# Kernel optimization log

Hardware: AMD Instinct MI355X
Metric: run time of the kernel (lower is better)

Reference implementation:

```python
import jax, jax.numpy as jnp
import numpy as np

N = 100000   # nodes
E = 400000   # edges
G = 1024     # graphs in batch
IN = 4; H = 128; HD = 4; DH = H // HD; L = 3; ED = 4; FF = 2 * H; JK = H * L
SCALE = 1.0 / np.sqrt(DH).astype(np.float32)


def _ln(x, g, b):
    m = x.mean(-1, keepdims=True)
    v = x.var(-1, keepdims=True)
    return (x - m) / jnp.sqrt(v + 1e-5) * g + b


def setup_inputs() -> dict:
    key = jax.random.key(0)
    ks = jax.random.split(key, 24)
    rn = lambda k, s, sc=0.05: jax.random.normal(k, s, jnp.float32) * sc
    return {
        "x": rn(ks[0], (N, IN), 1.0),
        "edge_index": jax.random.randint(ks[1], (2, E), 0, N),
        "edge_attr": rn(ks[2], (E, ED), 1.0),
        "batch": jnp.sort(jax.random.randint(ks[3], (N,), 0, G)),
        "u": rn(ks[4], (G, 1), 1.0),
        "Win": rn(ks[5], (IN, H)), "b_in": jnp.zeros(H),
        "Wq": rn(ks[6], (L, H, H)), "bq": jnp.zeros((L, H)),
        "Wk": rn(ks[7], (L, H, H)), "bk": jnp.zeros((L, H)),
        "Wv": rn(ks[8], (L, H, H)), "bv": jnp.zeros((L, H)),
        "We": rn(ks[9], (L, ED, H)),
        "Wskip": rn(ks[10], (L, H, H)), "bskip": jnp.zeros((L, H)),
        "ln1_g": jnp.ones((L, H)), "ln1_b": jnp.zeros((L, H)),
        "Wf1": rn(ks[11], (L, H, FF)), "bf1": jnp.zeros((L, FF)),
        "Wf2": rn(ks[12], (L, FF, H)), "bf2": jnp.zeros((L, H)),
        "ln2_g": jnp.ones((L, H)), "ln2_b": jnp.zeros((L, H)),
        "Wg1": rn(ks[13], (JK, H)), "bg1": jnp.zeros(H),
        "Wg2": rn(ks[14], (H, 1)), "bg2": jnp.zeros(1),
        "Wh1": rn(ks[15], (JK + 1, H)), "bh1": jnp.zeros(H),
        "Wh2": rn(ks[16], (H, 3)), "bh2": jnp.zeros(3),
    }


def reference(x, edge_index, edge_attr, batch, u,
              Win, b_in, Wq, bq, Wk, bk, Wv, bv, We, Wskip, bskip,
              ln1_g, ln1_b, Wf1, bf1, Wf2, bf2, ln2_g, ln2_b,
              Wg1, bg1, Wg2, bg2, Wh1, bh1, Wh2, bh2):
    src, dst = edge_index[0], edge_index[1]
    h = x @ Win + b_in                                   # [N,H]
    xs = []
    for l in range(L):
        q = (h @ Wq[l] + bq[l]).reshape(N, HD, DH)
        k_n = h @ Wk[l] + bk[l]
        v_n = h @ Wv[l] + bv[l]
        e = edge_attr @ We[l]                            # [E,H] edge bias
        ke = (k_n[src] + e).reshape(E, HD, DH)
        ve = (v_n[src] + e).reshape(E, HD, DH)
        logits = (q[dst] * ke).sum(-1) * SCALE           # [E,HD]
        m = jax.ops.segment_max(logits, dst, N)
        p = jnp.exp(logits - m[dst])
        s = jax.ops.segment_sum(p, dst, N)
        alpha = p / (s[dst] + 1e-16)                     # segment softmax per dst node
        agg = jax.ops.segment_sum(alpha[:, :, None] * ve, dst, N).reshape(N, H)
        attn = agg + h @ Wskip[l] + bskip[l]             # root weight (skip lin)
        h = _ln(h + attn, ln1_g[l], ln1_b[l])
        ff = jax.nn.relu(h @ Wf1[l] + bf1[l]) @ Wf2[l] + bf2[l]
        h = _ln(h + ff, ln2_g[l], ln2_b[l])
        xs.append(h)
    xc = jnp.concatenate(xs, -1)                         # JumpingKnowledge 'cat' [N,JK]
    gate = (jax.nn.relu(xc @ Wg1 + bg1) @ Wg2 + bg2)[:, 0]  # [N]
    gm = jax.ops.segment_max(gate, batch, G)
    gp = jnp.exp(gate - gm[batch])
    gs = jax.ops.segment_sum(gp, batch, G)
    w = gp / (gs[batch] + 1e-16)                         # per-graph softmax
    pooled = jax.ops.segment_sum(w[:, None] * xc, batch, G)  # [G,JK]
    out = jnp.concatenate([pooled, u], 1)                # [G,JK+1]
    return jax.nn.relu(out @ Wh1 + bh1) @ Wh2 + bh2      # [G,3]
```

## Files before the change

### kernel.cpp

```cpp
#include <hip/hip_runtime.h>
#include <math.h>

#define H 128
#define LAYERS 3
#define FFDIM 256
#define JK 384
#define ATT_SCALE 0.17677669529663687f

typedef unsigned short u16;
typedef __attribute__((ext_vector_type(4))) float f32x4;
typedef __attribute__((ext_vector_type(8))) short short8;
typedef __attribute__((ext_vector_type(8))) unsigned short ushort8v;

static inline int cdiv(int a, int b) { return (a + b - 1) / b; }

static __device__ __forceinline__ float bf2f(u16 u) {
    union { unsigned int i; float f; } v; v.i = ((unsigned int)u) << 16; return v.f;
}
static __device__ __forceinline__ u16 f2bf(float f) {
    union { float f; unsigned int i; } v; v.f = f;
    unsigned int r = v.i + 0x7FFFu + ((v.i >> 16) & 1u);
    return (u16)(r >> 16);
}

__global__ void hist_kernel(const int* __restrict__ ei, int* __restrict__ counts, int E) {
    int e = blockIdx.x * blockDim.x + threadIdx.x;
    if (e >= E) return;
    atomicAdd(&counts[ei[E + e]], 1);
}

__global__ __launch_bounds__(256) void scan1_kernel(const int* __restrict__ counts,
                                                    int* __restrict__ offsets,
                                                    int* __restrict__ bsum, int N) {
    __shared__ int sh[256];
    int t = threadIdx.x;
    int base = blockIdx.x * 1024 + t * 4;
    int v0 = 0, v1 = 0, v2 = 0, v3 = 0;
    if (base + 3 < N) {
        int4 q = *(const int4*)&counts[base];
        v0 = q.x; v1 = q.y; v2 = q.z; v3 = q.w;
    } else {
        if (base < N) v0 = counts[base];
        if (base + 1 < N) v1 = counts[base + 1];
        if (base + 2 < N) v2 = counts[base + 2];
        if (base + 3 < N) v3 = counts[base + 3];
    }
    int ts = v0 + v1 + v2 + v3;
    sh[t] = ts; __syncthreads();
    for (int off = 1; off < 256; off <<= 1) {
        int x = (t >= off) ? sh[t - off] : 0;
        __syncthreads(); sh[t] += x; __syncthreads();
    }
    int excl = sh[t] - ts;
    if (base < N)     offsets[base]     = excl;
    if (base + 1 < N) offsets[base + 1] = excl + v0;
    if (base + 2 < N) offsets[base + 2] = excl + v0 + v1;
    if (base + 3 < N) offsets[base + 3] = excl + v0 + v1 + v2;
    if (t == 255) bsum[blockIdx.x] = sh[255];
}

__global__ __launch_bounds__(128) void scan2_kernel(const int* __restrict__ bsum,
                                                    int* __restrict__ boffs,
                                                    int* __restrict__ offsets, int nb, int N) {
    __shared__ int sh[128];
    int t = threadIdx.x;
    int s = (t < nb) ? bsum[t] : 0;
    sh[t] = s; __syncthreads();
    for (int off = 1; off < 128; off <<= 1) {
        int x = (t >= off) ? sh[t - off] : 0;
        __syncthreads(); sh[t] += x; __syncthreads();
    }
    if (t < nb) boffs[t] = sh[t] - s;
    if (t == 0) offsets[N] = sh[nb - 1];
}

__global__ __launch_bounds__(256) void scan3_kernel(int* __restrict__ offsets,
                                                    const int* __restrict__ boffs, int N) {
    int add = boffs[blockIdx.x];
    int base = blockIdx.x * 1024 + threadIdx.x * 4;
#pragma unroll
    for (int i = 0; i < 4; ++i)
        if (base + i < N) offsets[base + i] += add;
}

__global__ void scatter_kernel(const int* __restrict__ ei, const float* __restrict__ eattr,
                               const int* __restrict__ offsets,
                               int* __restrict__ cursor, int* __restrict__ psrc,
                               float4* __restrict__ pe, int E) {
    int e = blockIdx.x * blockDim.x + threadIdx.x;
    if (e >= E) return;
    int d = ei[E + e];
    int pos = atomicAdd(&cursor[d], 1);
    int o = offsets[d] + pos;
    psrc[o] = ei[e];
    pe[o] = *(const float4*)&eattr[(size_t)e * 4];
}

__global__ void graph_bounds_kernel(const int* __restrict__ batch, int* __restrict__ gstart,
                                    int N, int G) {
    int g = blockIdx.x * blockDim.x + threadIdx.x;
    if (g > G) return;
    int lo = 0, hi = N;
    while (lo < hi) { int mid = (lo + hi) >> 1; if (batch[mid] < g) lo = mid + 1; else hi = mid; }
    gstart[g] = lo;
}

struct TD { const float* src; int dstoff, K, N; };
struct TA { TD d[19]; };

__global__ __launch_bounds__(256) void wconv_kernel(TA a, u16* __restrict__ WT) {
    TD d = a.d[blockIdx.y];
    int i = blockIdx.x * 256 + threadIdx.x;
    int tot = d.K * d.N;
    if (i >= tot) return;
    int c = i / d.K, k = i - c * d.K;
    WT[d.dstoff + i] = f2bf(d.src[(size_t)k * d.N + c]);
}

__global__ __launch_bounds__(256) void input_proj_kernel(const float* __restrict__ x,
                                                         const float* __restrict__ Win,
                                                         const float* __restrict__ b_in,
                                                         u16* __restrict__ h, int ldh, int N) {
    int idx = blockIdx.x * 256 + threadIdx.x;
    int n = idx >> 6, c = (idx & 63) * 2;
    if (n >= N) return;
    float4 xv = *(const float4*)&x[(size_t)n * 4];
    float o0 = b_in[c]     + xv.x * Win[c]     + xv.y * Win[H + c]     + xv.z * Win[2 * H + c]     + xv.w * Win[3 * H + c];
    float o1 = b_in[c + 1] + xv.x * Win[c + 1] + xv.y * Win[H + c + 1] + xv.z * Win[2 * H + c + 1] + xv.w * Win[3 * H + c + 1];
    ushort2 s; s.x = f2bf(o0); s.y = f2bf(o1);
    *(ushort2*)&h[(size_t)n * ldh + c] = s;
}

__device__ __forceinline__ void stage_tile(const u16* __restrict__ g, int ld, int row0,
                                           int nrows, int kt, u16* __restrict__ sm, int t) {
#pragma unroll
    for (int i = 0; i < 4; ++i) {
        int f = i * 256 + t;
        int row = f >> 3, ck = f & 7;
        int n = row0 + row; if (n >= nrows) n = nrows - 1;
        uint4 v = *(const uint4*)(g + (size_t)n * ld + kt + ck * 8);
        int sw = ck ^ (row & 7);
        *(uint4*)(sm + row * 64 + sw * 8) = v;
    }
}

template <int MODE, int NBY>
__global__ __launch_bounds__(256) void gemm_mfma(
    const u16* __restrict__ A, int lda,
    const u16* __restrict__ WT, int K,
    const float* __restrict__ b0, const float* __restrict__ b1,
    const float* __restrict__ b2, const float* __restrict__ b3,
    const u16* __restrict__ resid16,
    u16* __restrict__ obf, u16* __restrict__ obf2, float* __restrict__ of32,
    int nrows)
{
    alignas(16) __shared__ char smemraw[33792];
    u16* Asm = (u16*)smemraw;
    u16* Bsm = (u16*)(smemraw + 16384);
    float* stage = (float*)smemraw;
    int t = threadIdx.x;
    int lane = t & 63, wid = t >> 6;
    int wr = wid >> 1, wc = wid & 1;

    int T = gridDim.x, id = blockIdx.x;
    int qd = T >> 3, rr = T & 7;
    int xcd = id & 7, pos = id >> 3;
    int swz = (xcd < rr ? xcd * (qd + 1) : rr * (qd + 1) + (xcd - rr) * qd) + pos;
    int by = swz & (NBY - 1);
    int row0 = (swz / NBY) * 128;

    const u16* WTb = WT + (size_t)by * 128 * K;

    f32x4 acc[4][4] = {};

    for (int kt = 0; kt < K; kt += 64) {
        stage_tile(A, lda, row0, nrows, kt, Asm, t);
        stage_tile(WTb, K, 0, 128, kt, Bsm, t);
        __syncthreads();
        int g = lane >> 4;
        int l15 = lane & 15;
#pragma unroll
        for (int kk = 0; kk < 2; ++kk) {
            int cb = kk * 4 + g;
            short8 af[4], bf[4];
#pragma unroll
            for (int mi = 0; mi < 4; ++mi) {
                int r = wr * 64 + mi * 16 + l15;
                af[mi] = *(const short8*)(Asm + r * 64 + ((cb ^ (r & 7)) * 8));
            }
#pragma unroll
            for (int nj = 0; nj < 4; ++nj) {
                int c = wc * 64 + nj * 16 + l15;
                bf[nj] = *(const short8*)(Bsm + c * 64 + ((cb ^ (c & 7)) * 8));
            }
#pragma unroll
            for (int mi = 0; mi < 4; ++mi)
#pragma unroll
                for (int nj = 0; nj < 4; ++nj)
                    acc[mi][nj] = __builtin_amdgcn_mfma_f32_16x16x32_bf16(af[mi], bf[nj], acc[mi][nj], 0, 0, 0);
        }
        __syncthreads();
    }

    int g = lane >> 4, l15 = lane & 15;

    if (MODE == 3) {
        float* gsum = (float*)Asm;
        float part[4][4];
#pragma unroll
        for (int mi = 0; mi < 4; ++mi)
#pragma unroll
            for (int r = 0; r < 4; ++r) part[mi][r] = 0.f;
#pragma unroll
        for (int nj = 0; nj < 4; ++nj) {
            int col = wc * 64 + nj * 16 + l15;
            float bb = b0[col];
            float w2 = b1[col];
#pragma unroll
            for (int mi = 0; mi < 4; ++mi)
#pragma unroll
                for (int r = 0; r < 4; ++r) {
                    float v = fmaxf(acc[mi][nj][r] + bb, 0.f);
                    part[mi][r] = fmaf(v, w2, part[mi][r]);
                }
        }
#pragma unroll
        for (int off = 1; off <= 8; off <<= 1)
#pragma unroll
            for (int mi = 0; mi < 4; ++mi)
#pragma unroll
                for (int r = 0; r < 4; ++r) part[mi][r] += __shfl_xor(part[mi][r], off);
        if (wc == 0 && l15 == 0) {
#pragma unroll
            for (int mi = 0; mi < 4; ++mi)
#pragma unroll
                for (int r = 0; r < 4; ++r)
                    gsum[wr * 64 + mi * 16 + g * 4 + r] = part[mi][r];
        }
        __syncthreads();
        if (wc == 1 && l15 == 0) {
            float bg2v = b2[0];
#pragma unroll
            for (int mi = 0; mi < 4; ++mi)
#pragma unroll
                for (int r = 0; r < 4; ++r) {
                    int lr = wr * 64 + mi * 16 + g * 4 + r;
                    int n = row0 + lr;
                    if (n < nrows) of32[n] = part[mi][r] + gsum[lr] + bg2v;
                }
        }
        return;
    }

    const float* bias;
    u16* ob = nullptr; int ldob = 384; float* of = nullptr;
    if (MODE == 0) {
        bias = (by == 0) ? b0 : (by == 1) ? b1 : (by == 2) ? b2 : b3;
        if (by < 3) ob = obf + by * 128;
        else { ob = obf2; ldob = 128; }
    } else if (MODE == 1) {
        bias = b0 + by * 128;
        ob = obf + by * 128;
    } else {
        bias = b0;
        of = of32;
    }

#pragma unroll
    for (int p = 0; p < 2; ++p) {
        if (wr == p) {
#pragma unroll
            for (int nj = 0; nj < 4; ++nj) {
                int col = wc * 64 + nj * 16 + l15;
                float bb = bias[col];
#pragma unroll
                for (int mi = 0; mi < 4; ++mi)
#pragma unroll
                    for (int r = 0; r < 4; ++r) {
                        float v = acc[mi][nj][r] + bb;
                        if (MODE == 1) v = fmaxf(v, 0.f);
                        stage[(mi * 16 + g * 4 + r) * 132 + col] = v;
                    }
            }
        }
        __syncthreads();
        if (ob) {
#pragma unroll
            for (int it = 0; it < 4; ++it) {
                int lr = it * 16 + (t >> 4);
                int gr = row0 + p * 64 + lr;
                if (gr < nrows) {
                    int c8 = l15 * 8;
                    ushort8v o;
#pragma unroll
                    for (int i = 0; i < 8; ++i) o[i] = f2bf(stage[lr * 132 + c8 + i]);
                    *(ushort8v*)&ob[(size_t)gr * ldob + c8] = o;
                }
            }
        } else {
            int l31 = t & 31;
#pragma unroll
            for (int it = 0; it < 8; ++it) {
                int lr = it * 8 + (t >> 5);
                int gr = row0 + p * 64 + lr;
                if (gr < nrows) {
                    int c4 = l31 * 4;
                    float4 v = *(float4*)&stage[lr * 132 + c4];
                    if (MODE == 2) {
                        ushort4 rv = *(const ushort4*)&resid16[(size_t)gr * 384 + c4];
                        v.x += bf2f(rv.x); v.y += bf2f(rv.y); v.z += bf2f(rv.z); v.w += bf2f(rv.w);
                    }
                    *(float4*)&of[(size_t)gr * 128 + c4] = v;
                }
            }
        }
        __syncthreads();
    }
}

__global__ __launch_bounds__(256) void attn_kernel(
    u16* __restrict__ qkv,
    const u16* __restrict__ h_in, int ld_h,
    const u16* __restrict__ skipb,
    const int* __restrict__ offsets,
    const int* __restrict__ psrc, const float4* __restrict__ pe,
    const float* __restrict__ We_l,
    const float* __restrict__ g1, const float* __restrict__ b1,
    int N)
{
    int tid = threadIdx.x;
    int grp = tid >> 4;
    int sub = tid & 15;
    int n = blockIdx.x * 16 + grp;
    if (n >= N) return;
    int d0 = sub * 8;

    float we[4][8];
#pragma unroll
    for (int aa = 0; aa < 4; ++aa) {
        float4 w0 = *(const float4*)&We_l[aa * H + d0];
        float4 w1 = *(const float4*)&We_l[aa * H + d0 + 4];
        we[aa][0] = w0.x; we[aa][1] = w0.y; we[aa][2] = w0.z; we[aa][3] = w0.w;
        we[aa][4] = w1.x; we[aa][5] = w1.y; we[aa][6] = w1.z; we[aa][7] = w1.w;
    }

    ushort8v qraw = *(const ushort8v*)&qkv[(size_t)n * JK + d0];
    float qf[8];
#pragma unroll
    for (int i = 0; i < 8; ++i) qf[i] = bf2f(qraw[i]);

    float qe[4];
#pragma unroll
    for (int aa = 0; aa < 4; ++aa) {
        float s = 0.f;
#pragma unroll
        for (int i = 0; i < 8; ++i) s = fmaf(qf[i], we[aa][i], s);
        s += __shfl_xor(s, 1);
        s += __shfl_xor(s, 2);
        qe[aa] = s;
    }

    float m = -INFINITY, ssum = 0.f;
    float a[8] = {0.f, 0.f, 0.f, 0.f, 0.f, 0.f, 0.f, 0.f};
    float ws0 = 0.f, ws1 = 0.f, ws2 = 0.f, ws3 = 0.f;
    int e0 = offsets[n], e1 = offsets[n + 1];
    for (int j = e0; j < e1; ++j) {
        int s = psrc[j];
        float4 ea = pe[j];
        const u16* srow = qkv + (size_t)s * JK;
        ushort8v kraw = *(const ushort8v*)&srow[H + d0];
        ushort8v vraw = *(const ushort8v*)&srow[2 * H + d0];
        float part = 0.f;
#pragma unroll
        for (int i = 0; i < 8; ++i) part = fmaf(qf[i], bf2f(kraw[i]), part);
        part += __shfl_xor(part, 1);
        part += __shfl_xor(part, 2);
        float logit = (part + ea.x * qe[0] + ea.y * qe[1] + ea.z * qe[2] + ea.w * qe[3]) * ATT_SCALE;
        float mn = fmaxf(m, logit);
        float corr = __expf(m - mn);
        float p = __expf(logit - mn);
        ssum = ssum * corr + p;
#pragma unroll
        for (int i = 0; i < 8; ++i) a[i] = a[i] * corr + p * bf2f(vraw[i]);
        ws0 = ws0 * corr + p * ea.x;
        ws1 = ws1 * corr + p * ea.y;
        ws2 = ws2 * corr + p * ea.z;
        ws3 = ws3 * corr + p * ea.w;
        m = mn;
    }
    float inv = 1.f / (ssum + 1e-16f);
#pragma unroll
    for (int i = 0; i < 8; ++i)
        a[i] += ws0 * we[0][i] + ws1 * we[1][i] + ws2 * we[2][i] + ws3 * we[3][i];

    ushort8v hraw = *(const ushort8v*)&h_in[(size_t)n * ld_h + d0];
    ushort8v skraw = *(const ushort8v*)&skipb[(size_t)n * H + d0];
    float tv[8], sum = 0.f, sq = 0.f;
#pragma unroll
    for (int i = 0; i < 8; ++i) {
        tv[i] = bf2f(hraw[i]) + a[i] * inv + bf2f(skraw[i]);
        sum += tv[i]; sq += tv[i] * tv[i];
    }
#pragma unroll
    for (int off = 1; off <= 8; off <<= 1) { sum += __shfl_xor(sum, off); sq += __shfl_xor(sq, off); }
    float mean = sum * (1.f / 128.f);
    float var = sq * (1.f / 128.f) - mean * mean;
    float rstd = rsqrtf(var + 1e-5f);
    float4 ga = *(const float4*)&g1[d0];
    float4 gb = *(const float4*)&g1[d0 + 4];
    float4 ba = *(const float4*)&b1[d0];
    float4 bb = *(const float4*)&b1[d0 + 4];
    float gg[8] = {ga.x, ga.y, ga.z, ga.w, gb.x, gb.y, gb.z, gb.w};
    float bbv[8] = {ba.x, ba.y, ba.z, ba.w, bb.x, bb.y, bb.z, bb.w};
    ushort8v obv;
#pragma unroll
    for (int i = 0; i < 8; ++i)
        obv[i] = f2bf((tv[i] - mean) * rstd * gg[i] + bbv[i]);
    *(ushort8v*)&qkv[(size_t)n * JK + d0] = obv;
}

__global__ __launch_bounds__(256) void ln_kernel(const float* __restrict__ in,
                                                 const float* __restrict__ g,
                                                 const float* __restrict__ b,
                                                 u16* __restrict__ out, int ldo, int N) {
    int wid = threadIdx.x >> 6;
    int lane = threadIdx.x & 63;
    int n = blockIdx.x * 4 + wid;
    if (n >= N) return;
    int d0 = lane * 2;
    float2 t = *(const float2*)&in[(size_t)n * H + d0];
    float sum = t.x + t.y, sq = t.x * t.x + t.y * t.y;
#pragma unroll
    for (int off = 32; off; off >>= 1) { sum += __shfl_xor(sum, off); sq += __shfl_xor(sq, off); }
    float mean = sum * (1.f / 128.f);
    float var = sq * (1.f / 128.f) - mean * mean;
    float rstd = rsqrtf(var + 1e-5f);
    ushort2 s;
    s.x = f2bf((t.x - mean) * rstd * g[d0] + b[d0]);
    s.y = f2bf((t.y - mean) * rstd * g[d0 + 1] + b[d0 + 1]);
    *(ushort2*)&out[(size_t)n * ldo + d0] = s;
}

#define PCH 512
__global__ __launch_bounds__(256) void pool_kernel(const float* __restrict__ gate,
                                                   const u16* __restrict__ xc,
                                                   const int* __restrict__ gstart,
                                                   const float* __restrict__ u,
                                                   float* __restrict__ pooled, int G) {
    int g = blockIdx.x;
    int t = threadIdx.x;
    int s0 = gstart[g], s1 = gstart[g + 1];
    __shared__ float red[256];
    __shared__ float w[PCH];
    float mx = -INFINITY;
    for (int i = s0 + t; i < s1; i += 256) mx = fmaxf(mx, gate[i]);
    red[t] = mx; __syncthreads();
    for (int off = 128; off; off >>= 1) { if (t < off) red[t] = fmaxf(red[t], red[t + off]); __syncthreads(); }
    float gm = red[0]; __syncthreads();
    float sm = 0.f;
    for (int i = s0 + t; i < s1; i += 256) sm += __expf(gate[i] - gm);
    red[t] = sm; __syncthreads();
    for (int off = 128; off; off >>= 1) { if (t < off) red[t] += red[t + off]; __syncthreads(); }
    float inv = 1.f / (red[0] + 1e-16f);
    float acc0 = 0.f, acc1 = 0.f;
    for (int base = s0; base < s1; base += PCH) {
        int cnt = min(PCH, s1 - base);
        __syncthreads();
        for (int i = t; i < cnt; i += 256) w[i] = __expf(gate[base + i] - gm) * inv;
        __syncthreads();
        for (int c = 0; c < cnt; ++c) {
            const u16* row = xc + (size_t)(base + c) * JK;
            float wc = w[c];
            acc0 = fmaf(wc, bf2f(row[t]), acc0);
            if (t < 128) acc1 = fmaf(wc, bf2f(row[t + 256]), acc1);
        }
    }
    pooled[(size_t)g * (JK + 1) + t] = acc0;
    if (t < 128) pooled[(size_t)g * (JK + 1) + t + 256] = acc1;
    if (t == 0) pooled[(size_t)g * (JK + 1) + JK] = u[g];
}

__global__ __launch_bounds__(128) void head_kernel(const float* __restrict__ pooled,
                                                   const float* __restrict__ Wh1,
                                                   const float* __restrict__ bh1,
                                                   const float* __restrict__ Wh2,
                                                   const float* __restrict__ bh2,
                                                   float* __restrict__ out, int G) {
    int g = blockIdx.x;
    int j = threadIdx.x;
    __shared__ float hid[128];
    float acc = bh1[j];
    const float* pr = pooled + (size_t)g * (JK + 1);
    for (int k = 0; k < JK + 1; ++k) acc = fmaf(pr[k], Wh1[(size_t)k * H + j], acc);
    hid[j] = fmaxf(acc, 0.f);
    __syncthreads();
    if (j < 3) {
        float o = bh2[j];
        for (int k = 0; k < H; ++k) o += hid[k] * Wh2[k * 3 + j];
        out[(size_t)g * 3 + j] = o;
    }
}

extern "C" void kernel_launch(void* const* d_in, const int* in_sizes, int n_in,
                              void* d_out, int out_size, void* d_ws, size_t ws_size,
                              hipStream_t stream) {
    const float* x     = (const float*)d_in[0];
    const int*   ei    = (const int*)d_in[1];
    const float* eattr = (const float*)d_in[2];
    const int*   batch = (const int*)d_in[3];
    const float* u     = (const float*)d_in[4];
    const float* Win   = (const float*)d_in[5];
    const float* b_in  = (const float*)d_in[6];
    const float* Wq    = (const float*)d_in[7];
    const float* bq    = (const float*)d_in[8];
    const float* Wk    = (const float*)d_in[9];
    const float* bk    = (const float*)d_in[10];
    const float* Wv    = (const float*)d_in[11];
    const float* bv    = (const float*)d_in[12];
    const float* We    = (const float*)d_in[13];
    const float* Wskip = (const float*)d_in[14];
    const float* bskip = (const float*)d_in[15];
    const float* ln1_g = (const float*)d_in[16];
    const float* ln1_b = (const float*)d_in[17];
    const float* Wf1   = (const float*)d_in[18];
    const float* bf1   = (const float*)d_in[19];
    const float* Wf2   = (const float*)d_in[20];
    const float* bf2   = (const float*)d_in[21];
    const float* ln2_g = (const float*)d_in[22];
    const float* ln2_b = (const float*)d_in[23];
    const float* Wg1   = (const float*)d_in[24];
    const float* bg1   = (const float*)d_in[25];
    const float* Wg2   = (const float*)d_in[26];
    const float* bg2   = (const float*)d_in[27];
    const float* Wh1   = (const float*)d_in[28];
    const float* bh1   = (const float*)d_in[29];
    const float* Wh2   = (const float*)d_in[30];
    const float* bh2   = (const float*)d_in[31];

    const int N = in_sizes[3];
    const int E = in_sizes[1] / 2;
    const int G = in_sizes[4];

    char* p = (char*)d_ws;
    auto alloc = [&](size_t bytes) { char* r = p; p += (bytes + 255) & ~(size_t)255; return r; };
    int*    counts  = (int*)alloc((size_t)N * 4);
    int*    cursor  = (int*)alloc((size_t)N * 4);
    int*    offsets = (int*)alloc((size_t)(N + 1) * 4);
    int*    psrc    = (int*)alloc((size_t)E * 4);
    float4* pe      = (float4*)alloc((size_t)E * 16);
    int*    gstart  = (int*)alloc((size_t)(G + 1) * 4);
    int*    bsum    = (int*)alloc(128 * 4);
    int*    boffs   = (int*)alloc(128 * 4);
    float*  gate    = (float*)alloc((size_t)N * 4);
    float*  pooled  = (float*)alloc((size_t)G * (JK + 1) * 4);
    u16*    WT      = (u16*)alloc((size_t)442368 * 2);
    float*  hmid    = (float*)alloc((size_t)N * H * 4);
    u16*    skipb   = (u16*)hmid;
    u16*    xc      = (u16*)alloc((size_t)N * JK * 2);
    u16*    qkv     = (u16*)alloc((size_t)N * JK * 2);

    const int QKVS_OFF = 0;
    const int F1_OFF   = 3 * 65536;
    const int F2_OFF   = F1_OFF + 3 * 32768;
    const int G1_OFF   = F2_OFF + 3 * 32768;

    hipMemsetAsync(counts, 0, (size_t)N * 4, stream);
    hipMemsetAsync(cursor, 0, (size_t)N * 4, stream);

    int eb = cdiv(E, 256);
    int nb = cdiv(N, 1024);
    hist_kernel<<<eb, 256, 0, stream>>>(ei, counts, E);
    scan1_kernel<<<nb, 256, 0, stream>>>(counts, offsets, bsum, N);
    scan2_kernel<<<1, 128, 0, stream>>>(bsum, boffs, offsets, nb, N);
    scan3_kernel<<<nb, 256, 0, stream>>>(offsets, boffs, N);
    scatter_kernel<<<eb, 256, 0, stream>>>(ei, eattr, offsets, cursor, psrc, pe, E);
    graph_bounds_kernel<<<cdiv(G + 1, 256), 256, 0, stream>>>(batch, gstart, N, G);

    TA ta;
    for (int l = 0; l < 3; ++l) {
        ta.d[l * 4 + 0] = { Wq    + (size_t)l * 16384, QKVS_OFF + l * 65536 + 0,     128, 128 };
        ta.d[l * 4 + 1] = { Wk    + (size_t)l * 16384, QKVS_OFF + l * 65536 + 16384, 128, 128 };
        ta.d[l * 4 + 2] = { Wv    + (size_t)l * 16384, QKVS_OFF + l * 65536 + 32768, 128, 128 };
        ta.d[l * 4 + 3] = { Wskip + (size_t)l * 16384, QKVS_OFF + l * 65536 + 49152, 128, 128 };
        ta.d[12 + l]    = { Wf1   + (size_t)l * 32768, F1_OFF   + l * 32768,         128, 256 };
        ta.d[15 + l]    = { Wf2   + (size_t)l * 32768, F2_OFF   + l * 32768,         256, 128 };
    }
    ta.d[18] = { Wg1, G1_OFF, 384, 128 };
    dim3 wg(cdiv(49152, 256), 19);
    wconv_kernel<<<wg, 256, 0, stream>>>(ta, WT);

    input_proj_kernel<<<cdiv(N * 64, 256), 256, 0, stream>>>(x, Win, b_in, xc, JK, N);

    int gb = cdiv(N, 128);
    int nb16 = cdiv(N, 16);
    int nb4 = cdiv(N, 4);
    for (int l = 0; l < LAYERS; ++l) {
        const u16* hin = xc + (size_t)((l == 0) ? 0 : (l - 1) * H);
        gemm_mfma<0, 4><<<gb * 4, 256, 0, stream>>>(
            hin, JK, WT + QKVS_OFF + (size_t)l * 65536, 128,
            bq + l * H, bk + l * H, bv + l * H, bskip + l * H,
            nullptr, qkv, skipb, nullptr, N);
        attn_kernel<<<nb16, 256, 0, stream>>>(qkv, hin, JK, skipb, offsets, psrc, pe,
                                              We + (size_t)l * 4 * H, ln1_g + l * H, ln1_b + l * H,
                                              N);
        gemm_mfma<1, 2><<<gb * 2, 256, 0, stream>>>(
            qkv, JK, WT + F1_OFF + (size_t)l * 32768, 128,
            bf1 + (size_t)l * FFDIM, nullptr, nullptr, nullptr,
            nullptr, qkv + H, nullptr, nullptr, N);
        gemm_mfma<2, 1><<<gb, 256, 0, stream>>>(
            qkv + H, JK, WT + F2_OFF + (size_t)l * 32768, 256,
            bf2 + (size_t)l * H, nullptr, nullptr, nullptr,
            qkv, nullptr, nullptr, hmid, N);
        ln_kernel<<<nb4, 256, 0, stream>>>(hmid, ln2_g + l * H, ln2_b + l * H,
                                           xc + (size_t)l * H, JK, N);
    }

    gemm_mfma<3, 1><<<gb, 256, 0, stream>>>(
        xc, JK, WT + G1_OFF, JK,
        bg1, Wg2, bg2, nullptr,
        nullptr, nullptr, nullptr, gate, N);
    pool_kernel<<<G, 256, 0, stream>>>(gate, xc, gstart, u, pooled, G);
    head_kernel<<<G, 128, 0, stream>>>(pooled, Wh1, bh1, Wh2, bh2, (float*)d_out, G);
}
```

Baseline: 702.1 us.

## Fuse LayerNorm into FF2 GEMM epilogue, degree-sort attention nodes, prefetch edges

Three changes. The second LayerNorm is folded into the epilogue of the FF2 GEMM, which drops the fp32 hmid buffer and the separate ln_kernel round trip. The attention kernel now walks nodes in an order bucketed by in-degree, built by new histogram, scan and scatter kernels, so the 16 node groups in a block have similar loop lengths. The edge loop also software-prefetches the next edge's K/V rows; the degree permutation costs three small extra launches and may scatter the output writes more.

```diff
diff --git a/kernel.cpp b/kernel.cpp
--- a/kernel.cpp
+++ b/kernel.cpp
@@ -94,6 +94,34 @@
     int o = offsets[d] + pos;
     psrc[o] = ei[e];
     pe[o] = *(const float4*)&eattr[(size_t)e * 4];
+}
+
+__global__ void dhist_kernel(const int* __restrict__ counts, int* __restrict__ dhist, int N) {
+    int n = blockIdx.x * blockDim.x + threadIdx.x;
+    if (n >= N) return;
+    atomicAdd(&dhist[min(counts[n], 63)], 1);
+}
+
+__global__ __launch_bounds__(64) void dscan_kernel(const int* __restrict__ dhist,
+                                                   int* __restrict__ dstart) {
+    __shared__ int sh[64];
+    int t = threadIdx.x;
+    int s = dhist[t];
+    sh[t] = s; __syncthreads();
+    for (int off = 1; off < 64; off <<= 1) {
+        int x = (t >= off) ? sh[t - off] : 0;
+        __syncthreads(); sh[t] += x; __syncthreads();
+    }
+    dstart[t] = sh[t] - s;
+}
+
+__global__ void dscatter_kernel(const int* __restrict__ counts, const int* __restrict__ dstart,
+                                int* __restrict__ dcur, int* __restrict__ nperm, int N) {
+    int n = blockIdx.x * blockDim.x + threadIdx.x;
+    if (n >= N) return;
+    int b = min(counts[n], 63);
+    int pos = atomicAdd(&dcur[b], 1);
+    nperm[dstart[b] + pos] = n;
 }
 
 __global__ void graph_bounds_kernel(const int* __restrict__ batch, int* __restrict__ gstart,
@@ -253,7 +281,7 @@
     }
 
     const float* bias;
-    u16* ob = nullptr; int ldob = 384; float* of = nullptr;
+    u16* ob = nullptr; int ldob = 384;
     if (MODE == 0) {
         bias = (by == 0) ? b0 : (by == 1) ? b1 : (by == 2) ? b2 : b3;
         if (by < 3) ob = obf + by * 128;
@@ -263,7 +291,7 @@
         ob = obf + by * 128;
     } else {
         bias = b0;
-        of = of32;
+        ob = obf;
     }
 
 #pragma unroll
@@ -284,7 +312,37 @@
             }
         }
         __syncthreads();
-        if (ob) {
+        if (MODE == 2) {
+            int sub2 = t & 15, rowg = t >> 4;
+#pragma unroll
+            for (int it = 0; it < 4; ++it) {
+                int lr = it * 16 + rowg;
+                int gr = row0 + p * 64 + lr;
+                bool ok = gr < nrows;
+                int c8 = sub2 * 8;
+                float tv[8]; float sum = 0.f, sq = 0.f;
+                if (ok) {
+                    ushort8v rv = *(const ushort8v*)&resid16[(size_t)gr * 384 + c8];
+#pragma unroll
+                    for (int i = 0; i < 8; ++i) {
+                        tv[i] = stage[lr * 132 + c8 + i] + bf2f(rv[i]);
+                        sum += tv[i]; sq += tv[i] * tv[i];
+                    }
+                }
+#pragma unroll
+                for (int off = 1; off <= 8; off <<= 1) { sum += __shfl_xor(sum, off); sq += __shfl_xor(sq, off); }
+                if (ok) {
+                    float mean = sum * (1.f / 128.f);
+                    float var = sq * (1.f / 128.f) - mean * mean;
+                    float rstd = rsqrtf(var + 1e-5f);
+                    ushort8v o;
+#pragma unroll
+                    for (int i = 0; i < 8; ++i)
+                        o[i] = f2bf((tv[i] - mean) * rstd * b1[c8 + i] + b2[c8 + i]);
+                    *(ushort8v*)&ob[(size_t)gr * 384 + c8] = o;
+                }
+            }
+        } else {
 #pragma unroll
             for (int it = 0; it < 4; ++it) {
                 int lr = it * 16 + (t >> 4);
@@ -297,22 +355,6 @@
                     *(ushort8v*)&ob[(size_t)gr * ldob + c8] = o;
                 }
             }
-        } else {
-            int l31 = t & 31;
-#pragma unroll
-            for (int it = 0; it < 8; ++it) {
-                int lr = it * 8 + (t >> 5);
-                int gr = row0 + p * 64 + lr;
-                if (gr < nrows) {
-                    int c4 = l31 * 4;
-                    float4 v = *(float4*)&stage[lr * 132 + c4];
-                    if (MODE == 2) {
-                        ushort4 rv = *(const ushort4*)&resid16[(size_t)gr * 384 + c4];
-                        v.x += bf2f(rv.x); v.y += bf2f(rv.y); v.z += bf2f(rv.z); v.w += bf2f(rv.w);
-                    }
-                    *(float4*)&of[(size_t)gr * 128 + c4] = v;
-                }
-            }
         }
         __syncthreads();
     }
@@ -323,6 +365,7 @@
     const u16* __restrict__ h_in, int ld_h,
     const u16* __restrict__ skipb,
     const int* __restrict__ offsets,
+    const int* __restrict__ nperm,
     const int* __restrict__ psrc, const float4* __restrict__ pe,
     const float* __restrict__ We_l,
     const float* __restrict__ g1, const float* __restrict__ b1,
@@ -331,8 +374,9 @@
     int tid = threadIdx.x;
     int grp = tid >> 4;
     int sub = tid & 15;
-    int n = blockIdx.x * 16 + grp;
-    if (n >= N) return;
+    int idx = blockIdx.x * 16 + grp;
+    if (idx >= N) return;
+    int n = nperm[idx];
     int d0 = sub * 8;
 
     float we[4][8];
@@ -364,29 +408,40 @@
     float a[8] = {0.f, 0.f, 0.f, 0.f, 0.f, 0.f, 0.f, 0.f};
     float ws0 = 0.f, ws1 = 0.f, ws2 = 0.f, ws3 = 0.f;
     int e0 = offsets[n], e1 = offsets[n + 1];
-    for (int j = e0; j < e1; ++j) {
-        int s = psrc[j];
-        float4 ea = pe[j];
-        const u16* srow = qkv + (size_t)s * JK;
-        ushort8v kraw = *(const ushort8v*)&srow[H + d0];
-        ushort8v vraw = *(const ushort8v*)&srow[2 * H + d0];
-        float part = 0.f;
-#pragma unroll
-        for (int i = 0; i < 8; ++i) part = fmaf(qf[i], bf2f(kraw[i]), part);
-        part += __shfl_xor(part, 1);
-        part += __shfl_xor(part, 2);
-        float logit = (part + ea.x * qe[0] + ea.y * qe[1] + ea.z * qe[2] + ea.w * qe[3]) * ATT_SCALE;
-        float mn = fmaxf(m, logit);
-        float corr = __expf(m - mn);
-        float p = __expf(logit - mn);
-        ssum = ssum * corr + p;
-#pragma unroll
-        for (int i = 0; i < 8; ++i) a[i] = a[i] * corr + p * bf2f(vraw[i]);
-        ws0 = ws0 * corr + p * ea.x;
-        ws1 = ws1 * corr + p * ea.y;
-        ws2 = ws2 * corr + p * ea.z;
-        ws3 = ws3 * corr + p * ea.w;
-        m = mn;
+    if (e0 < e1) {
+        int s0i = psrc[e0];
+        float4 ea = pe[e0];
+        const u16* sr = qkv + (size_t)s0i * JK;
+        ushort8v kr = *(const ushort8v*)&sr[H + d0];
+        ushort8v vr = *(const ushort8v*)&sr[2 * H + d0];
+        for (int j = e0; j < e1; ++j) {
+            float4 ea2; ushort8v kr2, vr2;
+            if (j + 1 < e1) {
+                int s2 = psrc[j + 1];
+                ea2 = pe[j + 1];
+                const u16* sr2 = qkv + (size_t)s2 * JK;
+                kr2 = *(const ushort8v*)&sr2[H + d0];
+                vr2 = *(const ushort8v*)&sr2[2 * H + d0];
+            }
+            float part = 0.f;
+#pragma unroll
+            for (int i = 0; i < 8; ++i) part = fmaf(qf[i], bf2f(kr[i]), part);
+            part += __shfl_xor(part, 1);
+            part += __shfl_xor(part, 2);
+            float logit = (part + ea.x * qe[0] + ea.y * qe[1] + ea.z * qe[2] + ea.w * qe[3]) * ATT_SCALE;
+            float mn = fmaxf(m, logit);
+            float corr = __expf(m - mn);
+            float p = __expf(logit - mn);
+            ssum = ssum * corr + p;
+#pragma unroll
+            for (int i = 0; i < 8; ++i) a[i] = a[i] * corr + p * bf2f(vr[i]);
+            ws0 = ws0 * corr + p * ea.x;
+            ws1 = ws1 * corr + p * ea.y;
+            ws2 = ws2 * corr + p * ea.z;
+            ws3 = ws3 * corr + p * ea.w;
+            m = mn;
+            kr = kr2; vr = vr2; ea = ea2;
+        }
     }
     float inv = 1.f / (ssum + 1e-16f);
 #pragma unroll
@@ -417,28 +472,6 @@
     for (int i = 0; i < 8; ++i)
         obv[i] = f2bf((tv[i] - mean) * rstd * gg[i] + bbv[i]);
     *(ushort8v*)&qkv[(size_t)n * JK + d0] = obv;
-}
-
-__global__ __launch_bounds__(256) void ln_kernel(const float* __restrict__ in,
-                                                 const float* __restrict__ g,
-                                                 const float* __restrict__ b,
-                                                 u16* __restrict__ out, int ldo, int N) {
-    int wid = threadIdx.x >> 6;
-    int lane = threadIdx.x & 63;
-    int n = blockIdx.x * 4 + wid;
-    if (n >= N) return;
-    int d0 = lane * 2;
-    float2 t = *(const float2*)&in[(size_t)n * H + d0];
-    float sum = t.x + t.y, sq = t.x * t.x + t.y * t.y;
-#pragma unroll
-    for (int off = 32; off; off >>= 1) { sum += __shfl_xor(sum, off); sq += __shfl_xor(sq, off); }
-    float mean = sum * (1.f / 128.f);
-    float var = sq * (1.f / 128.f) - mean * mean;
-    float rstd = rsqrtf(var + 1e-5f);
-    ushort2 s;
-    s.x = f2bf((t.x - mean) * rstd * g[d0] + b[d0]);
-    s.y = f2bf((t.y - mean) * rstd * g[d0 + 1] + b[d0 + 1]);
-    *(ushort2*)&out[(size_t)n * ldo + d0] = s;
 }
 
 #define PCH 512
@@ -548,14 +581,17 @@
     int*    offsets = (int*)alloc((size_t)(N + 1) * 4);
     int*    psrc    = (int*)alloc((size_t)E * 4);
     float4* pe      = (float4*)alloc((size_t)E * 16);
+    int*    nperm   = (int*)alloc((size_t)N * 4);
     int*    gstart  = (int*)alloc((size_t)(G + 1) * 4);
     int*    bsum    = (int*)alloc(128 * 4);
     int*    boffs   = (int*)alloc(128 * 4);
+    int*    dhist   = (int*)alloc(64 * 4);
+    int*    dstart  = (int*)alloc(64 * 4);
+    int*    dcur    = (int*)alloc(64 * 4);
     float*  gate    = (float*)alloc((size_t)N * 4);
     float*  pooled  = (float*)alloc((size_t)G * (JK + 1) * 4);
     u16*    WT      = (u16*)alloc((size_t)442368 * 2);
-    float*  hmid    = (float*)alloc((size_t)N * H * 4);
-    u16*    skipb   = (u16*)hmid;
+    u16*    skipb   = (u16*)alloc((size_t)N * H * 2);
     u16*    xc      = (u16*)alloc((size_t)N * JK * 2);
     u16*    qkv     = (u16*)alloc((size_t)N * JK * 2);
 
@@ -566,14 +602,20 @@
 
     hipMemsetAsync(counts, 0, (size_t)N * 4, stream);
     hipMemsetAsync(cursor, 0, (size_t)N * 4, stream);
+    hipMemsetAsync(dhist, 0, 64 * 4, stream);
+    hipMemsetAsync(dcur, 0, 64 * 4, stream);
 
     int eb = cdiv(E, 256);
     int nb = cdiv(N, 1024);
+    int nthb = cdiv(N, 256);
     hist_kernel<<<eb, 256, 0, stream>>>(ei, counts, E);
     scan1_kernel<<<nb, 256, 0, stream>>>(counts, offsets, bsum, N);
     scan2_kernel<<<1, 128, 0, stream>>>(bsum, boffs, offsets, nb, N);
     scan3_kernel<<<nb, 256, 0, stream>>>(offsets, boffs, N);
     scatter_kernel<<<eb, 256, 0, stream>>>(ei, eattr, offsets, cursor, psrc, pe, E);
+    dhist_kernel<<<nthb, 256, 0, stream>>>(counts, dhist, N);
+    dscan_kernel<<<1, 64, 0, stream>>>(dhist, dstart);
+    dscatter_kernel<<<nthb, 256, 0, stream>>>(counts, dstart, dcur, nperm, N);
     graph_bounds_kernel<<<cdiv(G + 1, 256), 256, 0, stream>>>(batch, gstart, N, G);
 
     TA ta;
@@ -593,14 +635,13 @@
 
     int gb = cdiv(N, 128);
     int nb16 = cdiv(N, 16);
-    int nb4 = cdiv(N, 4);
     for (int l = 0; l < LAYERS; ++l) {
         const u16* hin = xc + (size_t)((l == 0) ? 0 : (l - 1) * H);
         gemm_mfma<0, 4><<<gb * 4, 256, 0, stream>>>(
             hin, JK, WT + QKVS_OFF + (size_t)l * 65536, 128,
             bq + l * H, bk + l * H, bv + l * H, bskip + l * H,
             nullptr, qkv, skipb, nullptr, N);
-        attn_kernel<<<nb16, 256, 0, stream>>>(qkv, hin, JK, skipb, offsets, psrc, pe,
+        attn_kernel<<<nb16, 256, 0, stream>>>(qkv, hin, JK, skipb, offsets, nperm, psrc, pe,
                                               We + (size_t)l * 4 * H, ln1_g + l * H, ln1_b + l * H,
                                               N);
         gemm_mfma<1, 2><<<gb * 2, 256, 0, stream>>>(
@@ -609,10 +650,8 @@
             nullptr, qkv + H, nullptr, nullptr, N);
         gemm_mfma<2, 1><<<gb, 256, 0, stream>>>(
             qkv + H, JK, WT + F2_OFF + (size_t)l * 32768, 256,
-            bf2 + (size_t)l * H, nullptr, nullptr, nullptr,
-            qkv, nullptr, nullptr, hmid, N);
-        ln_kernel<<<nb4, 256, 0, stream>>>(hmid, ln2_g + l * H, ln2_b + l * H,
-                                           xc + (size_t)l * H, JK, N);
+            bf2 + (size_t)l * H, ln2_g + (size_t)l * H, ln2_b + (size_t)l * H, nullptr,
+            qkv, xc + (size_t)l * H, nullptr, nullptr, N);
     }
 
     gemm_mfma<3, 1><<<gb, 256, 0, stream>>>(
```

Result: slower. 1.461 ms (+108.0%).
